# Optimization experiments

Hardware: AMD Instinct MI355X
Metric: run time of the kernel (lower is better)

The kernel has to match this reference:

```python
import jax, jax.numpy as jnp
import numpy as np

NUM_GROUPS = 8
EPS = 1e-5


def setup_inputs() -> dict:
    key = jax.random.key(0)
    ks = jax.random.split(key, 3)
    B, C, H, W = 32, 256, 64, 64
    x = jax.random.normal(ks[0], (B, C, H, W), dtype=jnp.float32)
    gn_weight = jnp.ones((C,), dtype=jnp.float32)
    gn_bias = jnp.zeros((C,), dtype=jnp.float32)
    # 1x1 convs stored as [out_ch, in_ch] matrices (kernel dims squeezed)
    qkv_weight = jax.random.normal(ks[1], (3 * C, C), dtype=jnp.float32) * (1.0 / np.sqrt(C))
    qkv_bias = jnp.zeros((3 * C,), dtype=jnp.float32)
    proj_weight = jax.random.normal(ks[2], (C, C), dtype=jnp.float32) * (1.0 / np.sqrt(C))
    proj_bias = jnp.zeros((C,), dtype=jnp.float32)
    return {
        "x": x,
        "gn_weight": gn_weight,
        "gn_bias": gn_bias,
        "qkv_weight": qkv_weight,
        "qkv_bias": qkv_bias,
        "proj_weight": proj_weight,
        "proj_bias": proj_bias,
    }


def _group_norm(x, weight, bias):
    B, C, H, W = x.shape
    g = x.reshape(B, NUM_GROUPS, C // NUM_GROUPS, H, W)
    mean = g.mean(axis=(2, 3, 4), keepdims=True)
    var = g.var(axis=(2, 3, 4), keepdims=True)
    g = (g - mean) * jax.lax.rsqrt(var + EPS)
    x = g.reshape(B, C, H, W)
    return x * weight[None, :, None, None] + bias[None, :, None, None]


def reference(x, gn_weight, gn_bias, qkv_weight, qkv_bias, proj_weight, proj_bias):
    B, C, H, W = x.shape
    x_norm = _group_norm(x, gn_weight, gn_bias)
    # 1x1 conv C -> 3C: contraction over channel dim
    qkv = jnp.einsum('bchw,oc->bohw', x_norm, qkv_weight) + qkv_bias[None, :, None, None]
    qkv = qkv.reshape(B, 3, C, H * W)  # [B,3,C,HW]
    q, k, v = qkv[:, 0], qkv[:, 1], qkv[:, 2]  # each [B,C,HW]
    # channel attention: attn is [B,C,C], softmax over last (key-channel) dim
    scale = 1.0 / jnp.sqrt(jnp.asarray(C, dtype=x.dtype))
    scores = jnp.einsum('bcn,bdn->bcd', q, k) * scale
    attn = jax.nn.softmax(scores, axis=-1)
    out = jnp.einsum('bcd,bdn->bcn', attn, v).reshape(B, C, H, W)
    proj = jnp.einsum('bchw,oc->bohw', out, proj_weight) + proj_bias[None, :, None, None]
    return x + proj
```

## Files before the change

### kernel.cpp

```cpp
#include <hip/hip_runtime.h>


#define B_ 32
#define C_ 256
#define N_ 4096
#define GSIZE (32 * N_)
#define EPSV 1e-5f
#define SCALE 0.0625f

#define OFF_SC    0
#define OFF_SH    8192
#define OFF_RS    16384
#define OFF_RSP   24576
#define OFF_SQP   90112
#define OFF_RALL  155648
#define OFF_UV    180224
#define OFF_CV    212992
#define OFF_CONST 221184
#define OFF_WVT   229376
#define OFF_GH    262144
#define OFF_GL    1310720
#define OFF_AT    2359296
#define OFF_S16   4456448
#define OFF_GP    5505024
#define OFF_XH    13893632

typedef _Float16 half_t;
typedef half_t f16x8 __attribute__((ext_vector_type(8)));
typedef float f32x16 __attribute__((ext_vector_type(16)));

#define GLL16(gsrc, ldst)                                                   \
  __builtin_amdgcn_global_load_lds(                                         \
      (const __attribute__((address_space(1))) void*)(gsrc),                \
      (__attribute__((address_space(3))) void*)(ldst), 16, 0, 0)

__global__ __launch_bounds__(256) void conv2_k(const float* __restrict__ x,
                                               float* __restrict__ ws) {
  __shared__ float rsl[32], rql[32];
  int bid = blockIdx.x;
  int slice = bid >> 3, rg = bid & 7;
  int b = slice >> 3, ks = slice & 7;
  int t = threadIdx.x;
  int wv = t >> 6, lane = t & 63;
  int c = lane >> 3, sg = lane & 7;
  char* img = (char*)((half_t*)(ws + OFF_XH) + (size_t)slice * 131072);
  const float* xbase = x + (size_t)b * (C_ * (size_t)N_) + ks * 512;
#pragma unroll
  for (int it = 0; it < 8; ++it) {
    int row = rg * 32 + it * 4 + wv;
    const float* src = xbase + (size_t)row * N_ + lane * 8;
    float4 v0 = *(const float4*)src;
    float4 v1 = *(const float4*)(src + 4);
    float rs = v0.x + v0.y + v0.z + v0.w + v1.x + v1.y + v1.z + v1.w;
    float rq = v0.x * v0.x + v0.y * v0.y + v0.z * v0.z + v0.w * v0.w +
               v1.x * v1.x + v1.y * v1.y + v1.z * v1.z + v1.w * v1.w;
    union { half_t h[8]; uint4 u; } P;
    P.h[0] = (half_t)v0.x; P.h[1] = (half_t)v0.y;
    P.h[2] = (half_t)v0.z; P.h[3] = (half_t)v0.w;
    P.h[4] = (half_t)v1.x; P.h[5] = (half_t)v1.y;
    P.h[6] = (half_t)v1.z; P.h[7] = (half_t)v1.w;
    *(uint4*)(img + c * 32768 + row * 128 + ((sg ^ (row & 7)) << 4)) = P.u;
    rs += __shfl_xor(rs, 1); rq += __shfl_xor(rq, 1);
    rs += __shfl_xor(rs, 2); rq += __shfl_xor(rq, 2);
    rs += __shfl_xor(rs, 4); rq += __shfl_xor(rq, 4);
    rs += __shfl_xor(rs, 8); rq += __shfl_xor(rq, 8);
    rs += __shfl_xor(rs, 16); rq += __shfl_xor(rq, 16);
    rs += __shfl_xor(rs, 32); rq += __shfl_xor(rq, 32);
    if (lane == 0) { rsl[it * 4 + wv] = rs; rql[it * 4 + wv] = rq; }
  }
  __syncthreads();
  if (t < 32) {
    ws[OFF_RSP + (size_t)slice * 256 + rg * 32 + t] = rsl[t];
    ws[OFF_SQP + (size_t)slice * 256 + rg * 32 + t] = rql[t];
  }
}

__global__ __launch_bounds__(1024, 4) void gram_v10_k(float* __restrict__ ws) {
  __shared__ __align__(16) char hb[2][32768];
  int slice = blockIdx.x;
  int t = threadIdx.x;
  int lane = t & 63, w = t >> 6;
  int wm = w >> 2, wn = w & 3, r31 = lane & 31, hi = lane >> 5;
  const char* img = (const char*)((half_t*)(ws + OFF_XH) + (size_t)slice * 131072);
  f32x16 acc[2][2] = {};

#define G10_ISSUE(cc, buf)                                                 \
  {                                                                        \
    const char* srcb = img + (cc) * 32768 + w * 2048;                      \
    char* dstb = hb[buf] + w * 2048;                                       \
    GLL16(srcb + lane * 16, dstb);                                         \
    GLL16(srcb + 1024 + lane * 16, dstb + 1024);                           \
  }

  G10_ISSUE(0, 0);
  __syncthreads();
  for (int c = 0; c < 8; ++c) {
    if (c < 7) G10_ISSUE(c + 1, (c + 1) & 1);
    const char* bp = hb[c & 1];
    __builtin_amdgcn_s_setprio(1);
#pragma unroll
    for (int kk = 0; kk < 4; ++kk) {
      int sidx = kk * 2 + hi;
      f16x8 Af[2], Bf[2];
#pragma unroll
      for (int m = 0; m < 2; ++m) {
        int row = wm * 64 + m * 32 + r31;
        Af[m] = *(const f16x8*)(bp + row * 128 + ((sidx ^ (row & 7)) << 4));
      }
#pragma unroll
      for (int n = 0; n < 2; ++n) {
        int row = wn * 64 + n * 32 + r31;
        Bf[n] = *(const f16x8*)(bp + row * 128 + ((sidx ^ (row & 7)) << 4));
      }
#pragma unroll
      for (int m = 0; m < 2; ++m)
#pragma unroll
        for (int n = 0; n < 2; ++n)
          acc[m][n] = __builtin_amdgcn_mfma_f32_32x32x16_f16(Af[m], Bf[n], acc[m][n], 0, 0, 0);
    }
    __builtin_amdgcn_s_setprio(0);
    __syncthreads();
  }
  half_t* Gp = (half_t*)(ws + OFF_GP) + (size_t)slice * 65536;
#pragma unroll
  for (int m = 0; m < 2; ++m)
#pragma unroll
    for (int n = 0; n < 2; ++n)
#pragma unroll
      for (int r = 0; r < 16; ++r) {
        int gr = wm * 64 + m * 32 + (r & 3) + 8 * (r >> 2) + 4 * hi;
        int gc = wn * 64 + n * 32 + r31;
        Gp[gr * 256 + gc] = (half_t)acc[m][n][r];
      }
#undef G10_ISSUE
}

__global__ __launch_bounds__(256) void gsum2_k(float* __restrict__ ws) {
  int bx = blockIdx.x;
  int b = bx >> 6, seg = bx & 63;
  int e0 = seg * 1024 + threadIdx.x * 4;
  const half_t* Gp = (const half_t*)(ws + OFF_GP) + (size_t)b * 8 * 65536 + e0;
  float s[4] = {0.f, 0.f, 0.f, 0.f};
#pragma unroll
  for (int ks = 0; ks < 8; ++ks) {
    union { uint2 u; half_t h[4]; } P;
    P.u = *(const uint2*)(Gp + (size_t)ks * 65536);
#pragma unroll
    for (int i = 0; i < 4; ++i) s[i] += (float)P.h[i];
  }
  union { half_t h[4]; uint2 u; } H, L;
#pragma unroll
  for (int i = 0; i < 4; ++i) {
    H.h[i] = (half_t)s[i];
    L.h[i] = (half_t)(s[i] - (float)H.h[i]);
  }
  *(uint2*)((half_t*)(ws + OFF_GH) + (size_t)b * 65536 + e0) = H.u;
  *(uint2*)((half_t*)(ws + OFF_GL) + (size_t)b * 65536 + e0) = L.u;
}

__global__ __launch_bounds__(256) void prep2_k(const float* __restrict__ gw,
                                               const float* __restrict__ gb,
                                               const float* __restrict__ qkvw,
                                               float* __restrict__ ws) {
  int b = blockIdx.x, t = threadIdx.x;
  __shared__ float sL[256], qL[256], svecs[256], scrs[256], shsm[256];
  __shared__ float gmean[8], grstd[8];
  float s = 0.f, q = 0.f;
#pragma unroll
  for (int ks = 0; ks < 8; ++ks) {
    s += ws[OFF_RSP + (b * 8 + ks) * 256 + t];
    q += ws[OFF_SQP + (b * 8 + ks) * 256 + t];
  }
  ws[OFF_RS + b * 256 + t] = s;
  sL[t] = s; qL[t] = q;
  __syncthreads();
  if (t < 8) {
    float gs = 0.f, gq = 0.f;
    for (int i = 0; i < 32; ++i) { gs += sL[t * 32 + i]; gq += qL[t * 32 + i]; }
    float mean = gs * (1.f / GSIZE);
    float var = gq * (1.f / GSIZE) - mean * mean;
    gmean[t] = mean;
    grstd[t] = rsqrtf(var + EPSV);
  }
  __syncthreads();
  int g = t >> 5;
  float sc = grstd[g] * gw[t];
  float sh = gb[t] - gmean[g] * sc;
  ws[OFF_SC + b * 256 + t] = sc;
  ws[OFF_SH + b * 256 + t] = sh;
  svecs[t] = s * sc + 4096.f * sh;
  scrs[t] = s * sc;
  shsm[t] = sh;
  __syncthreads();
  {
    const float* r1 = qkvw + (size_t)t * 256;
    float rq = 0.f, uq = 0.f, vq = 0.f;
#pragma unroll 4
    for (int c = 0; c < 256; ++c) {
      float wv = r1[c];
      rq += wv * svecs[c]; uq += wv * scrs[c]; vq += wv * shsm[c];
    }
    ws[OFF_RALL + b * 768 + t] = rq;
    ws[OFF_UV + b * 1024 + t] = uq;
    ws[OFF_UV + b * 1024 + 256 + t] = vq;
  }
  {
    const float* r2 = qkvw + (size_t)(256 + t) * 256;
    float rk = 0.f, uk = 0.f, vk = 0.f;
#pragma unroll 4
    for (int c = 0; c < 256; ++c) {
      float wv = r2[c];
      rk += wv * svecs[c]; uk += wv * scrs[c]; vk += wv * shsm[c];
    }
    ws[OFF_RALL + b * 768 + 256 + t] = rk;
    ws[OFF_UV + b * 1024 + 512 + t] = uk;
    ws[OFF_UV + b * 1024 + 768 + t] = vk;
  }
}

__global__ __launch_bounds__(256) void wvt2_k(const float* __restrict__ qkvw,
                                              float* __restrict__ ws) {
  __shared__ float sm[64][68];
  int be = blockIdx.x * 64, bd = blockIdx.y * 64;
  int t = threadIdx.x;
#pragma unroll
  for (int i = 0; i < 4; ++i) {
    int f = t + i * 256;
    int row = f >> 4, c4 = f & 15;
    float4 v = *(const float4*)(qkvw + (size_t)(512 + bd + row) * 256 + be + c4 * 4);
    sm[row][c4 * 4 + 0] = v.x; sm[row][c4 * 4 + 1] = v.y;
    sm[row][c4 * 4 + 2] = v.z; sm[row][c4 * 4 + 3] = v.w;
  }
  __syncthreads();
  half_t* WVT = (half_t*)(ws + OFF_WVT);
#pragma unroll
  for (int i = 0; i < 4; ++i) {
    int f = t + i * 256;
    int el = f >> 4, d4 = (f & 15) * 4;
    union { half_t h[4]; uint2 u; } P;
#pragma unroll
    for (int k = 0; k < 4; ++k) P.h[k] = (half_t)sm[d4 + k][el];
    *(uint2*)(WVT + (size_t)(be + el) * 256 + bd + d4) = P.u;
  }
}

__global__ __launch_bounds__(256) void logits2_k(
    const float* __restrict__ qkvw, const float* __restrict__ qkvb,
    float* __restrict__ ws) {
  int b = blockIdx.y, r0 = blockIdx.x * 32;
  int t = threadIdx.x, lane = t & 63, w = t >> 6, r31 = lane & 31, hi = lane >> 5;
  __shared__ __align__(16) char GHL[32768];
  __shared__ __align__(16) char AHL[8192];
  __shared__ float T1s[32][257];
  __shared__ float scs[256];
  __shared__ float bk_s[256], rk_s[256], uk_s[256], vk_s[256];
  __shared__ float bq_s[32], rq_s[32], uq_s[32], vq_s[32];
  scs[t] = ws[OFF_SC + b * 256 + t];
  bk_s[t] = qkvb[256 + t];
  rk_s[t] = ws[OFF_RALL + b * 768 + 256 + t];
  uk_s[t] = ws[OFF_UV + b * 1024 + 512 + t];
  vk_s[t] = ws[OFF_UV + b * 1024 + 768 + t];
  if (t < 32) {
    bq_s[t] = qkvb[r0 + t];
    rq_s[t] = ws[OFF_RALL + b * 768 + r0 + t];
    uq_s[t] = ws[OFF_UV + b * 1024 + r0 + t];
    vq_s[t] = ws[OFF_UV + b * 1024 + 256 + r0 + t];
  }
  __syncthreads();
  const half_t* Gh = (const half_t*)(ws + OFF_GH) + (size_t)b * 65536;
  const half_t* Gl = (const half_t*)(ws + OFF_GL) + (size_t)b * 65536;
  f32x16 acc[2] = {};
  for (int k0 = 0; k0 < 256; k0 += 32) {
    {
      int row = t >> 3, c4 = t & 7;
      float4 v = *(const float4*)(qkvw + (size_t)(r0 + row) * 256 + k0 + c4 * 4);
      union { half_t h[4]; uint2 u; } H;
      H.h[0] = (half_t)(v.x * scs[k0 + c4 * 4 + 0]);
      H.h[1] = (half_t)(v.y * scs[k0 + c4 * 4 + 1]);
      H.h[2] = (half_t)(v.z * scs[k0 + c4 * 4 + 2]);
      H.h[3] = (half_t)(v.w * scs[k0 + c4 * 4 + 3]);
      int s8 = row & 7;
      *(uint2*)(AHL + row * 128 + (((c4 >> 1) ^ s8) * 16) + (c4 & 1) * 8) = H.u;
    }
    {
#pragma unroll
      for (int p = 0; p < 8; ++p) {
        int f = t + p * 256;
        int row = f >> 3, ko = f & 7;
        const half_t* src = (ko < 4) ? Gh : Gl;
        uint4 v = *(const uint4*)(src + (size_t)row * 256 + k0 + (ko & 3) * 8);
        *(uint4*)(GHL + row * 128 + ((ko ^ (row & 7)) * 16)) = v;
      }
    }
    __syncthreads();
#pragma unroll
    for (int kk = 0; kk < 2; ++kk) {
      int kb = kk * 32 + hi * 16;
      int arow = r31;
      f16x8 Aq = *(const f16x8*)(AHL + arow * 128 + (((kb >> 4) ^ (arow & 7)) * 16));
#pragma unroll
      for (int n = 0; n < 2; ++n) {
        int row = w * 64 + n * 32 + r31;
        int s8 = row & 7;
        f16x8 Bh = *(const f16x8*)(GHL + row * 128 + (((kb >> 4) ^ s8) * 16));
        f16x8 Bl = *(const f16x8*)(GHL + row * 128 + ((((kb >> 4) + 4) ^ s8) * 16));
        acc[n] = __builtin_amdgcn_mfma_f32_32x32x16_f16(Aq, Bh, acc[n], 0, 0, 0);
        acc[n] = __builtin_amdgcn_mfma_f32_32x32x16_f16(Aq, Bl, acc[n], 0, 0, 0);
      }
    }
    __syncthreads();
  }
#pragma unroll
  for (int n = 0; n < 2; ++n)
#pragma unroll
    for (int r = 0; r < 16; ++r)
      T1s[(r & 3) + 8 * (r >> 2) + 4 * hi][w * 64 + n * 32 + r31] = acc[n][r];
  __syncthreads();
  f32x16 acc2[2] = {};
  for (int k0 = 0; k0 < 256; k0 += 64) {
    {
      int row = t >> 3;
#pragma unroll
      for (int u = 0; u < 2; ++u) {
        int c4 = (t & 7) + u * 8;
        float vv[4];
#pragma unroll
        for (int j = 0; j < 4; ++j) vv[j] = T1s[row][k0 + c4 * 4 + j];
        union { half_t h[4]; uint2 u2; } H, L;
#pragma unroll
        for (int j = 0; j < 4; ++j) {
          half_t h = (half_t)vv[j];
          H.h[j] = h; L.h[j] = (half_t)(vv[j] - (float)h);
        }
        int s16 = row & 15;
        *(uint2*)(AHL + row * 256 + (((c4 >> 1) ^ s16) * 16) + (c4 & 1) * 8) = H.u2;
        *(uint2*)(AHL + row * 256 + ((((c4 >> 1) + 8) ^ s16) * 16) + (c4 & 1) * 8) = L.u2;
      }
    }
    {
#pragma unroll
      for (int p = 0; p < 16; ++p) {
        int f = t + p * 256;
        int row = f >> 4, c4 = f & 15;
        float4 v = *(const float4*)(qkvw + (size_t)(256 + row) * 256 + k0 + c4 * 4);
        union { half_t h[4]; uint2 u; } H;
        H.h[0] = (half_t)(v.x * scs[k0 + c4 * 4 + 0]);
        H.h[1] = (half_t)(v.y * scs[k0 + c4 * 4 + 1]);
        H.h[2] = (half_t)(v.z * scs[k0 + c4 * 4 + 2]);
        H.h[3] = (half_t)(v.w * scs[k0 + c4 * 4 + 3]);
        int slot = (c4 >> 1) ^ (row & 7);
        *(uint2*)(GHL + row * 128 + slot * 16 + (c4 & 1) * 8) = H.u;
      }
    }
    __syncthreads();
#pragma unroll
    for (int kk = 0; kk < 4; ++kk) {
      int kb = kk * 32 + hi * 16;
      int arow = r31;
      int s16 = arow & 15;
      f16x8 Ah = *(const f16x8*)(AHL + arow * 256 + (((kb >> 4) ^ s16) * 16));
      f16x8 Al = *(const f16x8*)(AHL + arow * 256 + ((((kb >> 4) + 8) ^ s16) * 16));
#pragma unroll
      for (int n = 0; n < 2; ++n) {
        int row = w * 64 + n * 32 + r31;
        f16x8 Bf = *(const f16x8*)(GHL + row * 128 + (((kb >> 4) ^ (row & 7)) * 16));
        acc2[n] = __builtin_amdgcn_mfma_f32_32x32x16_f16(Ah, Bf, acc2[n], 0, 0, 0);
        acc2[n] = __builtin_amdgcn_mfma_f32_32x32x16_f16(Al, Bf, acc2[n], 0, 0, 0);
      }
    }
    __syncthreads();
  }
#pragma unroll
  for (int n = 0; n < 2; ++n)
#pragma unroll
    for (int r = 0; r < 16; ++r) {
      int rr = (r & 3) + 8 * (r >> 2) + 4 * hi;
      int cc = w * 64 + n * 32 + r31;
      float v = acc2[n][r];
      float ukv = uk_s[cc] + 4096.f * vk_s[cc];
      v = (v + uq_s[rr] * vk_s[cc] + vq_s[rr] * ukv + bq_s[rr] * rk_s[cc] +
           bk_s[cc] * (rq_s[rr] + 4096.f * bq_s[rr])) * SCALE;
      T1s[rr][cc] = v;
    }
  __syncthreads();
  bk_s[t] = qkvb[512 + t];
  __syncthreads();
  {
    int row = t >> 3, ls = t & 7;
    float m = -1e30f;
#pragma unroll
    for (int i = 0; i < 32; ++i) m = fmaxf(m, T1s[row][ls + i * 8]);
    m = fmaxf(m, __shfl_xor(m, 1));
    m = fmaxf(m, __shfl_xor(m, 2));
    m = fmaxf(m, __shfl_xor(m, 4));
    float s = 0.f, cvp = 0.f;
#pragma unroll
    for (int i = 0; i < 32; ++i) {
      int col = ls + i * 8;
      float e = __expf(T1s[row][col] - m);
      T1s[row][col] = e;
      s += e;
      cvp += e * bk_s[col];
    }
    s += __shfl_xor(s, 1); s += __shfl_xor(s, 2); s += __shfl_xor(s, 4);
    cvp += __shfl_xor(cvp, 1); cvp += __shfl_xor(cvp, 2); cvp += __shfl_xor(cvp, 4);
    float inv = 1.f / s;
#pragma unroll
    for (int i = 0; i < 32; ++i) T1s[row][ls + i * 8] *= inv;
    if (ls == 0) ws[OFF_CV + b * 256 + r0 + row] = cvp * inv;
  }
  __syncthreads();
  {
    float* ATb = ws + OFF_AT + (size_t)b * 65536;
#pragma unroll
    for (int u = 0; u < 8; ++u) {
      float4 v = {T1s[u * 4 + 0][t], T1s[u * 4 + 1][t], T1s[u * 4 + 2][t],
                  T1s[u * 4 + 3][t]};
      *(float4*)(ATb + (size_t)t * 256 + r0 + u * 4) = v;
    }
  }
}

__global__ __launch_bounds__(256) void fused_s_k(const float* __restrict__ pw,
                                                 const float* __restrict__ pb,
                                                 float* __restrict__ ws) {
  int b = blockIdx.y, r0 = blockIdx.x * 32;
  int t = threadIdx.x, lane = t & 63, w = t >> 6, r31 = lane & 31, hi = lane >> 5;
  __shared__ __align__(16) char GHL[32768];
  __shared__ __align__(16) char AHL[8192];
  __shared__ float T1s[32][257];
  __shared__ float cvs[256], scv[256], shv[256];
  cvs[t] = ws[OFF_CV + b * 256 + t];
  scv[t] = ws[OFF_SC + b * 256 + t];
  shv[t] = ws[OFF_SH + b * 256 + t];
  __syncthreads();
  const float* ATb = ws + OFF_AT + (size_t)b * 65536;
  f32x16 acc[2] = {};
  for (int k0 = 0; k0 < 256; k0 += 64) {
    {
#pragma unroll
      for (int p = 0; p < 2; ++p) {
        int f = t + p * 256;
        int row = f >> 4, c4 = f & 15;
        float4 v = *(const float4*)(pw + (size_t)(r0 + row) * 256 + k0 + c4 * 4);
        union { half_t h[4]; uint2 u; } H;
        H.h[0] = (half_t)v.x; H.h[1] = (half_t)v.y;
        H.h[2] = (half_t)v.z; H.h[3] = (half_t)v.w;
        int slot = (c4 >> 1) ^ (row & 7);
        *(uint2*)(AHL + row * 128 + slot * 16 + (c4 & 1) * 8) = H.u;
      }
    }
    {
#pragma unroll
      for (int p = 0; p < 16; ++p) {
        int f = t + p * 256;
        int row = f >> 4, c4 = f & 15;
        float4 v = *(const float4*)(ATb + (size_t)row * 256 + k0 + c4 * 4);
        union { half_t h[4]; uint2 u; } H;
        H.h[0] = (half_t)v.x; H.h[1] = (half_t)v.y;
        H.h[2] = (half_t)v.z; H.h[3] = (half_t)v.w;
        int slot = (c4 >> 1) ^ (row & 7);
        *(uint2*)(GHL + row * 128 + slot * 16 + (c4 & 1) * 8) = H.u;
      }
    }
    __syncthreads();
#pragma unroll
    for (int kk = 0; kk < 4; ++kk) {
      int kb = kk * 32 + hi * 16;
      int arow = r31;
      f16x8 Af = *(const f16x8*)(AHL + arow * 128 + (((kb >> 4) ^ (arow & 7)) * 16));
#pragma unroll
      for (int n = 0; n < 2; ++n) {
        int row = w * 64 + n * 32 + r31;
        f16x8 Bf = *(const f16x8*)(GHL + row * 128 + (((kb >> 4) ^ (row & 7)) * 16));
        acc[n] = __builtin_amdgcn_mfma_f32_32x32x16_f16(Af, Bf, acc[n], 0, 0, 0);
      }
    }
    __syncthreads();
  }
#pragma unroll
  for (int n = 0; n < 2; ++n)
#pragma unroll
    for (int r = 0; r < 16; ++r)
      T1s[(r & 3) + 8 * (r >> 2) + 4 * hi][w * 64 + n * 32 + r31] = acc[n][r];
  __syncthreads();
  float cfull = 0.f;
  {
    int row = t >> 3, ls = t & 7;
    float a = 0.f;
#pragma unroll
    for (int i = 0; i < 32; ++i) {
      int c = ls + i * 8;
      a += pw[(size_t)(r0 + row) * 256 + c] * cvs[c];
    }
    a += __shfl_xor(a, 1); a += __shfl_xor(a, 2); a += __shfl_xor(a, 4);
    cfull = a + pb[r0 + row];
  }
  const half_t* WVT = (const half_t*)(ws + OFF_WVT);
  f32x16 acc2[2] = {};
  for (int k0 = 0; k0 < 256; k0 += 64) {
    {
      int row = t >> 3;
#pragma unroll
      for (int u = 0; u < 2; ++u) {
        int c4 = (t & 7) + u * 8;
        float vv[4];
#pragma unroll
        for (int j = 0; j < 4; ++j) vv[j] = T1s[row][k0 + c4 * 4 + j];
        union { half_t h[4]; uint2 u2; } H, L;
#pragma unroll
        for (int j = 0; j < 4; ++j) {
          half_t h = (half_t)vv[j];
          H.h[j] = h; L.h[j] = (half_t)(vv[j] - (float)h);
        }
        int s16 = row & 15;
        *(uint2*)(AHL + row * 256 + (((c4 >> 1) ^ s16) * 16) + (c4 & 1) * 8) = H.u2;
        *(uint2*)(AHL + row * 256 + ((((c4 >> 1) + 8) ^ s16) * 16) + (c4 & 1) * 8) = L.u2;
      }
    }
    {
#pragma unroll
      for (int p = 0; p < 8; ++p) {
        int f = t + p * 256;
        int row = f >> 3, h8 = f & 7;
        uint2 v = *(const uint2*)(WVT + (size_t)row * 256 + k0 + h8 * 8);
        uint2 v2 = *(const uint2*)(WVT + (size_t)row * 256 + k0 + h8 * 8 + 4);
        int slot = h8 ^ (row & 7);
        *(uint2*)(GHL + row * 128 + slot * 16) = v;
        *(uint2*)(GHL + row * 128 + slot * 16 + 8) = v2;
      }
    }
    __syncthreads();
#pragma unroll
    for (int kk = 0; kk < 4; ++kk) {
      int kb = kk * 32 + hi * 16;
      int arow = r31;
      int s16 = arow & 15;
      f16x8 Ah = *(const f16x8*)(AHL + arow * 256 + (((kb >> 4) ^ s16) * 16));
      f16x8 Al = *(const f16x8*)(AHL + arow * 256 + ((((kb >> 4) + 8) ^ s16) * 16));
#pragma unroll
      for (int n = 0; n < 2; ++n) {
        int row = w * 64 + n * 32 + r31;
        f16x8 Bf = *(const f16x8*)(GHL + row * 128 + (((kb >> 4) ^ (row & 7)) * 16));
        acc2[n] = __builtin_amdgcn_mfma_f32_32x32x16_f16(Ah, Bf, acc2[n], 0, 0, 0);
        acc2[n] = __builtin_amdgcn_mfma_f32_32x32x16_f16(Al, Bf, acc2[n], 0, 0, 0);
      }
    }
    __syncthreads();
  }
#pragma unroll
  for (int n = 0; n < 2; ++n)
#pragma unroll
    for (int r = 0; r < 16; ++r)
      T1s[(r & 3) + 8 * (r >> 2) + 4 * hi][w * 64 + n * 32 + r31] = acc2[n][r];
  __syncthreads();
  {
    half_t* Sb = (half_t*)(ws + OFF_S16) + (size_t)b * 65536;
    int row = t >> 3, seg = t & 7;
    float dsh = 0.f;
#pragma unroll
    for (int u = 0; u < 4; ++u) {
      union { half_t h[8]; uint4 v; } P;
#pragma unroll
      for (int j = 0; j < 8; ++j) {
        int col = seg * 32 + u * 8 + j;
        float sv = T1s[row][col];
        dsh += sv * shv[col];
        P.h[j] = (half_t)(sv * scv[col]);
      }
      *(uint4*)(Sb + (size_t)(r0 + row) * 256 + seg * 32 + u * 8) = P.v;
    }
    dsh += __shfl_xor(dsh, 1); dsh += __shfl_xor(dsh, 2); dsh += __shfl_xor(dsh, 4);
    if (seg == 0) ws[OFF_CONST + b * 256 + r0 + row] = cfull + dsh;
  }
}

__global__ __launch_bounds__(256, 4) void final_v5_k(
    const float* __restrict__ x, float* __restrict__ out,
    const float* __restrict__ ws) {
  __shared__ __align__(16) char xs[32768];
  int b = blockIdx.y, n0 = blockIdx.x * 64;
  int t = threadIdx.x, lane = t & 63, w = t >> 6;
  int r31 = lane & 31, hi = lane >> 5;
  const half_t* Sb = (const half_t*)(ws + OFF_S16) + (size_t)b * 65536;
  int slice = b * 8 + (n0 >> 9);
  int chunk = (n0 & 511) >> 6;
  const char* img = (const char*)((half_t*)(ws + OFF_XH) + (size_t)slice * 131072) +
                    chunk * 32768;
  {
    int n4 = (t & 15) * 4, cb = (t >> 4) * 4;
    int sgi = n4 >> 3, off8 = (n4 & 7) * 2;
#pragma unroll
    for (int p = 0; p < 4; ++p) {
      int c = cb + p * 64;
      union { uint2 u; unsigned short s[4]; } in[4];
#pragma unroll
      for (int i = 0; i < 4; ++i) {
        int row = c + i;
        in[i].u = *(const uint2*)(img + row * 128 + ((sgi ^ (row & 7)) << 4) + off8);
      }
#pragma unroll
      for (int j = 0; j < 4; ++j) {
        int n = n4 + j;
        union { unsigned short s[4]; uint2 u; } O;
        O.s[0] = in[0].s[j]; O.s[1] = in[1].s[j];
        O.s[2] = in[2].s[j]; O.s[3] = in[3].s[j];
        int g = ((cb >> 3) & 7) ^ ((n >> 3) & 7) ^ (n & 7);
        *(uint2*)(xs + p * 8192 + n * 128 + g * 16 + (cb & 7) * 2) = O.u;
      }
    }
  }
  __syncthreads();
  f32x16 acc[2][2] = {};
  int obase = w * 64;
  const half_t* Arow0 = Sb + (size_t)(obase + r31) * 256;
  const half_t* Arow1 = Sb + (size_t)(obase + 32 + r31) * 256;
  f16x8 An0[2], An1[2];
  An0[0] = *(const f16x8*)(Arow0 + hi * 8);
  An0[1] = *(const f16x8*)(Arow1 + hi * 8);
  An1[0] = *(const f16x8*)(Arow0 + 16 + hi * 8);
  An1[1] = *(const f16x8*)(Arow1 + 16 + hi * 8);
#pragma unroll
  for (int kk = 0; kk < 16; ++kk) {
    f16x8 Af[2];
    if (kk & 1) { Af[0] = An1[0]; Af[1] = An1[1]; }
    else        { Af[0] = An0[0]; Af[1] = An0[1]; }
    if (kk < 14) {
      int ck2 = (kk + 2) * 16 + hi * 8;
      if (kk & 1) { An1[0] = *(const f16x8*)(Arow0 + ck2); An1[1] = *(const f16x8*)(Arow1 + ck2); }
      else        { An0[0] = *(const f16x8*)(Arow0 + ck2); An0[1] = *(const f16x8*)(Arow1 + ck2); }
    }
    int ck = kk * 16 + hi * 8;
    int q = ck >> 6, ch = (ck >> 3) & 7;
    f16x8 Bf[2];
#pragma unroll
    for (int n = 0; n < 2; ++n) {
      int col = n * 32 + r31;
      int g = ch ^ ((col >> 3) & 7) ^ (col & 7);
      Bf[n] = *(const f16x8*)(xs + q * 8192 + col * 128 + g * 16);
    }
#pragma unroll
    for (int m = 0; m < 2; ++m)
#pragma unroll
      for (int n = 0; n < 2; ++n)
        acc[m][n] = __builtin_amdgcn_mfma_f32_32x32x16_f16(Af[m], Bf[n], acc[m][n], 0, 0, 0);
  }
  float* ob = out + (size_t)b * (C_ * (size_t)N_);
  const float* cstb = ws + OFF_CONST + b * 256;
#pragma unroll
  for (int m = 0; m < 2; ++m)
#pragma unroll
    for (int r = 0; r < 16; ++r) {
      int o = obase + m * 32 + (r & 3) + 8 * (r >> 2) + 4 * hi;
      float cv = cstb[o];
      size_t base = (size_t)o * N_ + n0;
      int q = o >> 6, ch = (o >> 3) & 7;
#pragma unroll
      for (int n = 0; n < 2; ++n) {
        int col = n * 32 + r31;
        int g = ch ^ ((col >> 3) & 7) ^ (col & 7);
        float xr = (float)*(const half_t*)(xs + q * 8192 + col * 128 + g * 16 + (o & 7) * 2);
        ob[base + col] = acc[m][n][r] + xr + cv;
      }
    }
}

extern "C" void kernel_launch(void* const* d_in, const int* in_sizes, int n_in,
                              void* d_out, int out_size, void* d_ws,
                              size_t ws_size, hipStream_t stream) {
  const float* x = (const float*)d_in[0];
  const float* gw = (const float*)d_in[1];
  const float* gb = (const float*)d_in[2];
  const float* qkvw = (const float*)d_in[3];
  const float* qkvb = (const float*)d_in[4];
  const float* pw = (const float*)d_in[5];
  const float* pb = (const float*)d_in[6];
  float* out = (float*)d_out;
  float* ws = (float*)d_ws;

  hipLaunchKernelGGL(conv2_k, dim3(2048), dim3(256), 0, stream, x, ws);
  hipLaunchKernelGGL(gram_v10_k, dim3(256), dim3(1024), 0, stream, ws);
  hipLaunchKernelGGL(prep2_k, dim3(32), dim3(256), 0, stream, gw, gb, qkvw, ws);
  hipLaunchKernelGGL(gsum2_k, dim3(2048), dim3(256), 0, stream, ws);
  hipLaunchKernelGGL(wvt2_k, dim3(4, 4), dim3(256), 0, stream, qkvw, ws);
  hipLaunchKernelGGL(logits2_k, dim3(8, 32), dim3(256), 0, stream, qkvw, qkvb, ws);
  hipLaunchKernelGGL(fused_s_k, dim3(8, 32), dim3(256), 0, stream, pw, pb, ws);
  hipLaunchKernelGGL(final_v5_k, dim3(64, 32), dim3(256), 0, stream, x, out, ws);
}
```

Before: 223.6 us.

## Pre-swizzle Gram image in gsum and double-buffer logits loads via global_load_lds

The Gram-sum kernel now writes its hi/lo fp16 halves straight into a pre-swizzled, per-k-chunk LDS image layout instead of two plain row-major arrays. The logits kernel then copies each 32-column chunk into shared memory with direct global-to-LDS loads, double-buffering both the Gram and A tiles so the next chunk's loads overlap the current chunk's MFMAs. This removes the register round trip and per-element address swizzling on the load path, at the cost of doubled LDS for the B buffer, which may reduce occupancy. The loop shown has no barrier after the MFMAs, so buffer reuse safety depends on code not visible here.

```diff
diff --git a/kernel.cpp b/kernel.cpp
--- a/kernel.cpp
+++ b/kernel.cpp
@@ -18,8 +18,7 @@
 #define OFF_CV    212992
 #define OFF_CONST 221184
 #define OFF_WVT   229376
-#define OFF_GH    262144
-#define OFF_GL    1310720
+#define OFF_GIMG  262144
 #define OFF_AT    2359296
 #define OFF_S16   4456448
 #define OFF_GP    5505024
@@ -135,7 +134,7 @@
 #undef G10_ISSUE
 }
 
-__global__ __launch_bounds__(256) void gsum2_k(float* __restrict__ ws) {
+__global__ __launch_bounds__(256) void gsum3_k(float* __restrict__ ws) {
   int bx = blockIdx.x;
   int b = bx >> 6, seg = bx & 63;
   int e0 = seg * 1024 + threadIdx.x * 4;
@@ -154,8 +153,13 @@
     H.h[i] = (half_t)s[i];
     L.h[i] = (half_t)(s[i] - (float)H.h[i]);
   }
-  *(uint2*)((half_t*)(ws + OFF_GH) + (size_t)b * 65536 + e0) = H.u;
-  *(uint2*)((half_t*)(ws + OFF_GL) + (size_t)b * 65536 + e0) = L.u;
+  int row = e0 >> 8, col = e0 & 255;
+  char* img = (char*)(ws + OFF_GIMG) + (size_t)b * 262144 +
+              (col >> 5) * 32768 + row * 128;
+  int sh_ = (col & 31) >> 3;
+  int half8 = ((col >> 2) & 1) * 8;
+  *(uint2*)(img + (((sh_) ^ (row & 7)) << 4) + half8) = H.u;
+  *(uint2*)(img + (((sh_ + 4) ^ (row & 7)) << 4) + half8) = L.u;
 }
 
 __global__ __launch_bounds__(256) void prep2_k(const float* __restrict__ gw,
@@ -244,12 +248,12 @@
   }
 }
 
-__global__ __launch_bounds__(256) void logits2_k(
+__global__ __launch_bounds__(256) void logits3_k(
     const float* __restrict__ qkvw, const float* __restrict__ qkvb,
     float* __restrict__ ws) {
   int b = blockIdx.y, r0 = blockIdx.x * 32;
   int t = threadIdx.x, lane = t & 63, w = t >> 6, r31 = lane & 31, hi = lane >> 5;
-  __shared__ __align__(16) char GHL[32768];
+  __shared__ __align__(16) char GB[2][32768];
   __shared__ __align__(16) char AHL[8192];
   __shared__ float T1s[32][257];
   __shared__ float scs[256];
@@ -266,44 +270,52 @@
     uq_s[t] = ws[OFF_UV + b * 1024 + r0 + t];
     vq_s[t] = ws[OFF_UV + b * 1024 + 256 + r0 + t];
   }
-  __syncthreads();
-  const half_t* Gh = (const half_t*)(ws + OFF_GH) + (size_t)b * 65536;
-  const half_t* Gl = (const half_t*)(ws + OFF_GL) + (size_t)b * 65536;
+  const char* Gimg = (const char*)(ws + OFF_GIMG) + (size_t)b * 262144;
+
+#define LG_ISSUE(cc, buf)                                                  \
+  {                                                                        \
+    const char* srcb = Gimg + (cc) * 32768 + w * 1024;                     \
+    char* dstb = GB[buf] + w * 1024;                                       \
+    _Pragma("unroll") for (int i = 0; i < 8; ++i)                          \
+        GLL16(srcb + i * 4096 + lane * 16, dstb + i * 4096);               \
+  }
+
+#define LG_STAGEA(k0, abuf)                                                \
+  {                                                                        \
+    int row = t >> 3, c4 = t & 7;                                          \
+    float4 v = *(const float4*)(qkvw + (size_t)(r0 + row) * 256 + (k0) + c4 * 4); \
+    union { half_t h[4]; uint2 u; } H;                                     \
+    H.h[0] = (half_t)(v.x * scs[(k0) + c4 * 4 + 0]);                       \
+    H.h[1] = (half_t)(v.y * scs[(k0) + c4 * 4 + 1]);                       \
+    H.h[2] = (half_t)(v.z * scs[(k0) + c4 * 4 + 2]);                       \
+    H.h[3] = (half_t)(v.w * scs[(k0) + c4 * 4 + 3]);                       \
+    int s8 = row & 7;                                                      \
+    *(uint2*)((abuf) + row * 128 + (((c4 >> 1) ^ s8) * 16) + (c4 & 1) * 8) = H.u; \
+  }
+
+  __syncthreads();
   f32x16 acc[2] = {};
-  for (int k0 = 0; k0 < 256; k0 += 32) {
-    {
-      int row = t >> 3, c4 = t & 7;
-      float4 v = *(const float4*)(qkvw + (size_t)(r0 + row) * 256 + k0 + c4 * 4);
-      union { half_t h[4]; uint2 u; } H;
-      H.h[0] = (half_t)(v.x * scs[k0 + c4 * 4 + 0]);
-      H.h[1] = (half_t)(v.y * scs[k0 + c4 * 4 + 1]);
-      H.h[2] = (half_t)(v.z * scs[k0 + c4 * 4 + 2]);
-      H.h[3] = (half_t)(v.w * scs[k0 + c4 * 4 + 3]);
-      int s8 = row & 7;
-      *(uint2*)(AHL + row * 128 + (((c4 >> 1) ^ s8) * 16) + (c4 & 1) * 8) = H.u;
-    }
-    {
-#pragma unroll
-      for (int p = 0; p < 8; ++p) {
-        int f = t + p * 256;
-        int row = f >> 3, ko = f & 7;
-        const half_t* src = (ko < 4) ? Gh : Gl;
-        uint4 v = *(const uint4*)(src + (size_t)row * 256 + k0 + (ko & 3) * 8);
-        *(uint4*)(GHL + row * 128 + ((ko ^ (row & 7)) * 16)) = v;
-      }
-    }
-    __syncthreads();
+  LG_ISSUE(0, 0);
+  LG_STAGEA(0, AHL);
+  __syncthreads();
+  for (int c = 0; c < 8; ++c) {
+    if (c < 7) {
+      LG_ISSUE(c + 1, (c + 1) & 1);
+      LG_STAGEA((c + 1) * 32, AHL + ((c + 1) & 1) * 4096);
+    }
+    const char* bp = GB[c & 1];
+    const char* ap = AHL + (c & 1) * 4096;
 #pragma unroll
     for (int kk = 0; kk < 2; ++kk) {
-      int kb = kk * 32 + hi * 16;
+      int sidx = kk * 2 + hi;
       int arow = r31;
-      f16x8 Aq = *(const f16x8*)(AHL + arow * 128 + (((kb >> 4) ^ (arow & 7)) * 16));
+      f16x8 Aq = *(const f16x8*)(ap + arow * 128 + ((sidx ^ (arow & 7)) << 4));
 #pragma unroll
       for (int n = 0; n < 2; ++n) {
         int row = w * 64 + n * 32 + r31;
         int s8 = row & 7;
-        f16x8 Bh = *(const f16x8*)(GHL + row * 128 + (((kb >> 4) ^ s8) * 16));
-        f16x8 Bl = *(const f16x8*)(GHL + row * 128 + ((((kb >> 4) + 4) ^ s8) * 16));
+        f16x8 Bh = *(const f16x8*)(bp + row * 128 + ((sidx ^ s8) << 4));
+        f16x8 Bl = *(const f16x8*)(bp + row * 128 + (((sidx + 4) ^ s8) << 4));
         acc[n] = __builtin_amdgcn_mfma_f32_32x32x16_f16(Aq, Bh, acc[n], 0, 0, 0);
         acc[n] = __builtin_amdgcn_mfma_f32_32x32x16_f16(Aq, Bl, acc[n], 0, 0, 0);
       }
@@ -349,7 +361,7 @@
         H.h[2] = (half_t)(v.z * scs[k0 + c4 * 4 + 2]);
         H.h[3] = (half_t)(v.w * scs[k0 + c4 * 4 + 3]);
         int slot = (c4 >> 1) ^ (row & 7);
-        *(uint2*)(GHL + row * 128 + slot * 16 + (c4 & 1) * 8) = H.u;
+        *(uint2*)(GB[0] + row * 128 + slot * 16 + (c4 & 1) * 8) = H.u;
       }
     }
     __syncthreads();
@@ -363,7 +375,7 @@
 #pragma unroll
       for (int n = 0; n < 2; ++n) {
         int row = w * 64 + n * 32 + r31;
-        f16x8 Bf = *(const f16x8*)(GHL + row * 128 + (((kb >> 4) ^ (row & 7)) * 16));
+        f16x8 Bf = *(const f16x8*)(GB[0] + row * 128 + (((kb >> 4) ^ (row & 7)) * 16));
         acc2[n] = __builtin_amdgcn_mfma_f32_32x32x16_f16(Ah, Bf, acc2[n], 0, 0, 0);
         acc2[n] = __builtin_amdgcn_mfma_f32_32x32x16_f16(Al, Bf, acc2[n], 0, 0, 0);
       }
@@ -419,6 +431,8 @@
       *(float4*)(ATb + (size_t)t * 256 + r0 + u * 4) = v;
     }
   }
+#undef LG_ISSUE
+#undef LG_STAGEA
 }
 
 __global__ __launch_bounds__(256) void fused_s_k(const float* __restrict__ pw,
@@ -681,9 +695,9 @@
   hipLaunchKernelGGL(conv2_k, dim3(2048), dim3(256), 0, stream, x, ws);
   hipLaunchKernelGGL(gram_v10_k, dim3(256), dim3(1024), 0, stream, ws);
   hipLaunchKernelGGL(prep2_k, dim3(32), dim3(256), 0, stream, gw, gb, qkvw, ws);
-  hipLaunchKernelGGL(gsum2_k, dim3(2048), dim3(256), 0, stream, ws);
+  hipLaunchKernelGGL(gsum3_k, dim3(2048), dim3(256), 0, stream, ws);
   hipLaunchKernelGGL(wvt2_k, dim3(4, 4), dim3(256), 0, stream, qkvw, ws);
-  hipLaunchKernelGGL(logits2_k, dim3(8, 32), dim3(256), 0, stream, qkvw, qkvb, ws);
+  hipLaunchKernelGGL(logits3_k, dim3(8, 32), dim3(256), 0, stream, qkvw, qkvb, ws);
   hipLaunchKernelGGL(fused_s_k, dim3(8, 32), dim3(256), 0, stream, pw, pb, ws);
   hipLaunchKernelGGL(final_v5_k, dim3(64, 32), dim3(256), 0, stream, x, out, ws);
 }
```

New measurement: 221.4 us. No clear change (-1.0%).
